# Optimization experiments

Hardware: AMD Instinct MI355X
Metric: run time of the kernel (lower is better)

Reference implementation:

```python
import jax, jax.numpy as jnp
import numpy as np

B, T, D, H, K = 4, 2048, 512, 8, 31
INNER = 2048  # dim * ff_mult
DH = D // H   # 64
EPS = 1e-5

def _ln(x, g, b):
    m = jnp.mean(x, axis=-1, keepdims=True)
    v = jnp.var(x, axis=-1, keepdims=True)
    return (x - m) * jax.lax.rsqrt(v + EPS) * g + b

def _ff(x, g, b, w1, b1, w2, b2):
    h = jax.nn.silu(_ln(x, g, b) @ w1 + b1)
    return h @ w2 + b2

def _rope_cos_sin(t, dh, theta=10000.0):
    freqs = 1.0 / theta ** (jnp.arange(0, dh, 2, dtype=jnp.float32) / dh)
    ang = jnp.arange(t, dtype=jnp.float32)[:, None] * freqs[None, :]
    return jnp.cos(ang), jnp.sin(ang)

def _rotate(x, cos, sin):
    # x: [B,T,H,DH]; complex rotation on (even, odd) pairs, matches torch view_as_complex
    xr = x.reshape(x.shape[:-1] + (DH // 2, 2))
    xe, xo = xr[..., 0], xr[..., 1]
    c, s = cos[None, :, None, :], sin[None, :, None, :]
    return jnp.stack([xe * c - xo * s, xe * s + xo * c], axis=-1).reshape(x.shape)

def setup_inputs():
    ks = iter(jax.random.split(jax.random.key(0), 16))
    w = lambda *s: jax.random.normal(next(ks), s, jnp.float32) * 0.02
    ones = lambda n: jnp.ones((n,), jnp.float32)
    zeros = lambda n: jnp.zeros((n,), jnp.float32)
    return dict(
        x=jax.random.normal(next(ks), (B, T, D), jnp.float32),
        ff1_lng=ones(D), ff1_lnb=zeros(D),
        ff1_w1=w(D, INNER), ff1_b1=zeros(INNER), ff1_w2=w(INNER, D), ff1_b2=zeros(D),
        attn_lng=ones(D), attn_lnb=zeros(D),
        wq=w(D, D), wk=w(D, D), wv=w(D, D), wo=w(D, D),
        conv_lng=ones(D), conv_lnb=zeros(D),
        pw1_w=w(D, 2 * D), pw1_b=zeros(2 * D),
        dw_w=w(D, K), dw_b=zeros(D),
        bn_g=ones(D), bn_b=zeros(D),
        pw2_w=w(D, D), pw2_b=zeros(D),
        ff2_lng=ones(D), ff2_lnb=zeros(D),
        ff2_w1=w(D, INNER), ff2_b1=zeros(INNER), ff2_w2=w(INNER, D), ff2_b2=zeros(D),
        out_lng=ones(D), out_lnb=zeros(D),
    )

def reference(x, ff1_lng, ff1_lnb, ff1_w1, ff1_b1, ff1_w2, ff1_b2,
              attn_lng, attn_lnb, wq, wk, wv, wo,
              conv_lng, conv_lnb, pw1_w, pw1_b, dw_w, dw_b, bn_g, bn_b, pw2_w, pw2_b,
              ff2_lng, ff2_lnb, ff2_w1, ff2_b1, ff2_w2, ff2_b2,
              out_lng, out_lnb):
    # ff1 half-step
    x = x + 0.5 * _ff(x, ff1_lng, ff1_lnb, ff1_w1, ff1_b1, ff1_w2, ff1_b2)
    # RoPE MHSA
    h = _ln(x, attn_lng, attn_lnb)
    q = (h @ wq).reshape(B, T, H, DH)
    k = (h @ wk).reshape(B, T, H, DH)
    v = (h @ wv).reshape(B, T, H, DH)
    cos, sin = _rope_cos_sin(T, DH)
    q, k = _rotate(q, cos, sin), _rotate(k, cos, sin)
    scores = jnp.einsum('bqhd,bkhd->bhqk', q, k) / np.float32(np.sqrt(DH))
    o = jnp.einsum('bhqk,bkhd->bqhd', jax.nn.softmax(scores, axis=-1), v).reshape(B, T, D)
    x = x + o @ wo
    # Conformer conv module
    h = _ln(x, conv_lng, conv_lnb) @ pw1_w + pw1_b         # pointwise1 -> [B,T,2D]
    h = h[..., :D] * jax.nn.sigmoid(h[..., D:])            # GLU over channels
    h = h.transpose(0, 2, 1)                               # [B,D,T]
    h = jax.lax.conv_general_dilated(h, dw_w[:, None, :], (1,), [(K // 2, K // 2)],
                                     dimension_numbers=('NCH', 'OIH', 'NCH'),
                                     feature_group_count=D) + dw_b[None, :, None]
    mu = jnp.mean(h, axis=(0, 2), keepdims=True)           # training-mode BatchNorm1d
    var = jnp.var(h, axis=(0, 2), keepdims=True)
    h = (h - mu) * jax.lax.rsqrt(var + EPS) * bn_g[None, :, None] + bn_b[None, :, None]
    h = jax.nn.silu(h).transpose(0, 2, 1) @ pw2_w + pw2_b  # pointwise2 -> [B,T,D]
    x = x + h
    # ff2 half-step + final LN
    x = x + 0.5 * _ff(x, ff2_lng, ff2_lnb, ff2_w1, ff2_b1, ff2_w2, ff2_b2)
    return _ln(x, out_lng, out_lnb)
```

## Files before the change

kernel.cpp:

```cpp
#include <hip/hip_runtime.h>


typedef float  f32x4   __attribute__((ext_vector_type(4)));
typedef float  f32x16  __attribute__((ext_vector_type(16)));
typedef __bf16 bf16_t;
typedef __bf16 bf16x8  __attribute__((ext_vector_type(8)));
typedef unsigned short u16;
typedef unsigned short u16x4 __attribute__((ext_vector_type(4)));
typedef unsigned short u16x8 __attribute__((ext_vector_type(8)));
typedef unsigned int   u32x4 __attribute__((ext_vector_type(4)));

#define DEVI __device__ __forceinline__

static constexpr int CB = 4, CT = 2048, CD = 512, CH = 8, CDH = 64, CINNER = 2048, CK = 31;
static constexpr int CBT = CB * CT;

DEVI u16 f2bf(float f) {
  unsigned u = __builtin_bit_cast(unsigned, f);
  u += 0x7FFFu + ((u >> 16) & 1u);
  return (u16)(u >> 16);
}
DEVI float bf2f(u16 h) { return __builtin_bit_cast(float, (unsigned)h << 16); }
DEVI float sigm(float x) { return 1.0f / (1.0f + __expf(-x)); }

DEVI unsigned cvtpk(float lo, float hi) {
  unsigned r;
  asm("v_cvt_pk_bf16_f32 %0, %1, %2" : "=v"(r) : "v"(lo), "v"(hi));
  return r;
}

DEVI void gload16(const bf16_t* g, bf16_t* l) {
  __builtin_amdgcn_global_load_lds(
      (const __attribute__((address_space(1))) unsigned int*)g,
      (__attribute__((address_space(3))) unsigned int*)l, 16, 0, 0);
}

DEVI void pipe_wait(int t, int nt) {
  if (t + 3 <= nt)      asm volatile("s_waitcnt vmcnt(12)" ::: "memory");
  else if (t + 2 == nt) asm volatile("s_waitcnt vmcnt(6)" ::: "memory");
  else                  asm volatile("s_waitcnt vmcnt(0)" ::: "memory");
}

enum { EPI_BF = 0, EPI_SILU_BF = 1, EPI_RES = 2, EPI_GLU = 3 };

template<int EPI>
__global__ __launch_bounds__(512) void gemm8(
    const bf16_t* __restrict__ A, const bf16_t* __restrict__ B,
    const float* __restrict__ bias, const float* __restrict__ res,
    void* __restrict__ Cv,
    int lda, int ldb, int ldc, int Kd, float scale)
{
  __shared__ __align__(16) bf16_t As[3][256 * 64];
  __shared__ __align__(16) bf16_t Bs[3][128 * 64];

  const int gx = gridDim.x;
  const int nwg = gx * gridDim.y;
  int wg = blockIdx.y * gx + blockIdx.x;
  wg = (wg & 7) * (nwg >> 3) + (wg >> 3);
  const int m0 = (wg / gx) * 256, n0 = (wg % gx) * 128;

  const int tid = threadIdx.x;
  const int wid = tid >> 6, lane = tid & 63;
  const int lrow = lane & 15, lk = lane >> 4;
  const int wm = (wid >> 1) * 64, wn = (wid & 1) * 64;
  const int r = tid >> 3;
  const int cs = (((tid & 7) ^ (r & 7)) << 3);
  const int fsw = lrow & 7;

  auto stage = [&](int kt, int s) {
    const bf16_t* ga = A + (long)(m0 + r) * lda + (kt * 64 + cs);
    const bf16_t* gb = B + (long)(n0 + r) * ldb + (kt * 64 + cs);
    bf16_t* as = &As[s][0];
    bf16_t* bs = &Bs[s][0];
#pragma unroll
    for (int it = 0; it < 4; ++it)
      gload16(ga + (long)it * 64 * lda, as + tid * 8 + it * 4096);
#pragma unroll
    for (int it = 0; it < 2; ++it)
      gload16(gb + (long)it * 64 * ldb, bs + tid * 8 + it * 4096);
  };

  f32x4 acc[4][4] = {};
  const int nt = Kd / 64;

  stage(0, 0);
  stage(1, 1);
  stage(2, 2);

  int s = 0;
  for (int t = 0; t < nt; ++t) {
    pipe_wait(t, nt);
    asm volatile("s_barrier" ::: "memory");

    bf16x8 av[2][4], bv[2][4];
    const bf16_t* as = &As[s][0];
    const bf16_t* bs = &Bs[s][0];
#pragma unroll
    for (int kk = 0; kk < 2; ++kk) {
#pragma unroll
      for (int i = 0; i < 4; ++i)
        av[kk][i] = *(const bf16x8*)&as[(wm + i * 16 + lrow) * 64 + ((((kk << 2) + lk) ^ fsw) << 3)];
#pragma unroll
      for (int j = 0; j < 4; ++j)
        bv[kk][j] = *(const bf16x8*)&bs[(wn + j * 16 + lrow) * 64 + ((((kk << 2) + lk) ^ fsw) << 3)];
    }
    __builtin_amdgcn_s_setprio(1);
#pragma unroll
    for (int kk = 0; kk < 2; ++kk)
#pragma unroll
      for (int i = 0; i < 4; ++i)
#pragma unroll
        for (int j = 0; j < 4; ++j)
          acc[i][j] = __builtin_amdgcn_mfma_f32_16x16x32_bf16(av[kk][i], bv[kk][j], acc[i][j], 0, 0, 0);
    __builtin_amdgcn_s_setprio(0);

    asm volatile("s_barrier" ::: "memory");
    if (t + 3 < nt) stage(t + 3, s);
    s = (s == 2) ? 0 : s + 1;
  }

  if constexpr (EPI == EPI_GLU) {
#pragma unroll
    for (int jp = 0; jp < 2; ++jp) {
      int oc = ((n0 + wn) >> 1) + jp * 16 + lrow;
      float ba = bias[oc], bb = bias[512 + oc];
#pragma unroll
      for (int i = 0; i < 4; ++i) {
#pragma unroll
        for (int rr = 0; rr < 4; ++rr) {
          int row = m0 + wm + i * 16 + lk * 4 + rr;
          float av_ = acc[i][2 * jp][rr] + ba;
          float bv_ = acc[i][2 * jp + 1][rr] + bb;
          ((bf16_t*)Cv)[(long)row * ldc + oc] = (bf16_t)(av_ * sigm(bv_));
        }
      }
    }
  } else {
#pragma unroll
    for (int j = 0; j < 4; ++j) {
      int col = n0 + wn + j * 16 + lrow;
      float bb = bias ? bias[col] : 0.0f;
#pragma unroll
      for (int i = 0; i < 4; ++i) {
#pragma unroll
        for (int rr = 0; rr < 4; ++rr) {
          int row = m0 + wm + i * 16 + lk * 4 + rr;
          long idx = (long)row * ldc + col;
          float v = (acc[i][j][rr] + bb) * scale;
          if constexpr (EPI == EPI_SILU_BF) v *= sigm(v);
          if constexpr (EPI == EPI_RES) {
            ((float*)Cv)[idx] = res[idx] + v;
          } else {
            ((bf16_t*)Cv)[idx] = (bf16_t)v;
          }
        }
      }
    }
  }
}

template<int BM, int BN, int BK, int EPI>
__global__ __launch_bounds__(256) void gemm_bf(
    const bf16_t* __restrict__ A, const bf16_t* __restrict__ B,
    const float* __restrict__ bias, const float* __restrict__ res,
    void* __restrict__ Cv,
    int lda, int ldb, int ldc, int Kd, float scale)
{
  __shared__ __align__(16) bf16_t As[BM * BK];
  __shared__ __align__(16) bf16_t Bs[BN * BK];

  const int gx = gridDim.x;
  const int nwg = gx * gridDim.y;
  int wg = blockIdx.y * gx + blockIdx.x;
  wg = (wg & 7) * (nwg >> 3) + (wg >> 3);
  const int m0 = (wg / gx) * BM, n0 = (wg % gx) * BN;

  const int tid = threadIdx.x;
  const int wid = tid >> 6, lane = tid & 63;
  const int lrow = lane & 15, lk = lane >> 4;
  constexpr int FM = BM / 32, FN = BN / 32;
  constexpr int NK = BK / 32;
  constexpr int TPR = BK / 8;
  constexpr int RPP = 256 / TPR;
  const int wm = (wid >> 1) * (BM / 2), wn = (wid & 1) * (BN / 2);
  const int r = tid / TPR;
  const int cs = (((tid & (TPR - 1)) ^ (r & 7)) << 3);
  const int fsw = lrow & 7;

  f32x4 acc[FM][FN] = {};

  for (int k0 = 0; k0 < Kd; k0 += BK) {
    const bf16_t* ga = A + (long)(m0 + r) * lda + (k0 + cs);
    const bf16_t* gb = B + (long)(n0 + r) * ldb + (k0 + cs);
#pragma unroll
    for (int it = 0; it < BM / RPP; ++it)
      gload16(ga + (long)it * RPP * lda, &As[tid * 8 + it * 2048]);
#pragma unroll
    for (int it = 0; it < BN / RPP; ++it)
      gload16(gb + (long)it * RPP * ldb, &Bs[tid * 8 + it * 2048]);
    __syncthreads();

    bf16x8 av[NK][FM], bv[NK][FN];
#pragma unroll
    for (int kk = 0; kk < NK; ++kk) {
#pragma unroll
      for (int i = 0; i < FM; ++i)
        av[kk][i] = *(const bf16x8*)&As[(wm + i * 16 + lrow) * BK + ((((kk << 2) + lk) ^ fsw) << 3)];
#pragma unroll
      for (int j = 0; j < FN; ++j)
        bv[kk][j] = *(const bf16x8*)&Bs[(wn + j * 16 + lrow) * BK + ((((kk << 2) + lk) ^ fsw) << 3)];
    }
#pragma unroll
    for (int kk = 0; kk < NK; ++kk)
#pragma unroll
      for (int i = 0; i < FM; ++i)
#pragma unroll
        for (int j = 0; j < FN; ++j)
          acc[i][j] = __builtin_amdgcn_mfma_f32_16x16x32_bf16(av[kk][i], bv[kk][j], acc[i][j], 0, 0, 0);
    __syncthreads();
  }

#pragma unroll
  for (int j = 0; j < FN; ++j) {
    int col = n0 + wn + j * 16 + lrow;
    float bb = bias ? bias[col] : 0.0f;
#pragma unroll
    for (int i = 0; i < FM; ++i) {
#pragma unroll
      for (int rr = 0; rr < 4; ++rr) {
        int row = m0 + wm + i * 16 + lk * 4 + rr;
        long idx = (long)row * ldc + col;
        float v = (acc[i][j][rr] + bb) * scale;
        if constexpr (EPI == EPI_SILU_BF) v *= sigm(v);
        if constexpr (EPI == EPI_RES) {
          ((float*)Cv)[idx] = res[idx] + v;
        } else {
          ((bf16_t*)Cv)[idx] = (bf16_t)v;
        }
      }
    }
  }
}

__global__ __launch_bounds__(256) void fattn_k(
    const bf16_t* __restrict__ QK,
    const bf16_t* __restrict__ VT,
    bf16_t* __restrict__ O)
{
  __shared__ __align__(16) bf16_t S[16384];

  const int tid = threadIdx.x;
  const int w = tid >> 6, lane = tid & 63;
  const int l31 = lane & 31, hi = lane >> 5;
  const int q0 = blockIdx.x * 128;
  const int bh = blockIdx.y, b = bh >> 3, h = bh & 7;

  const int r8 = tid >> 3;
  const int csw = ((tid & 7) ^ (r8 & 7)) << 3;
  const int fswl = l31 & 7;

  const bf16_t* Qg = QK + ((long)b * CT + q0) * 1536 + h * 64;
  const bf16_t* Kg = QK + (long)b * CT * 1536 + 512 + h * 64;
  const bf16_t* Vg = VT + (long)bh * 64 * 2048;

#pragma unroll
  for (int it = 0; it < 4; ++it)
    gload16(Qg + (long)(r8 + it * 32) * 1536 + csw, &S[8192 + tid * 8 + it * 2048]);
#pragma unroll
  for (int it = 0; it < 2; ++it)
    gload16(Kg + (long)(r8 + it * 32) * 1536 + csw, &S[tid * 8 + it * 2048]);
#pragma unroll
  for (int it = 0; it < 2; ++it)
    gload16(Vg + (long)(r8 + it * 32) * 2048 + csw, &S[4096 + tid * 8 + it * 2048]);
  __syncthreads();

  bf16x8 qb[4];
#pragma unroll
  for (int m = 0; m < 4; ++m)
    qb[m] = *(const bf16x8*)&S[8192 + (w * 32 + l31) * 64 + (((m * 2 + hi) ^ fswl) << 3)];
  __syncthreads();

  const u16x8 onesu = {0x3F80, 0x3F80, 0x3F80, 0x3F80, 0x3F80, 0x3F80, 0x3F80, 0x3F80};
  const bf16x8 onesf = __builtin_bit_cast(bf16x8, onesu);

  f32x16 o0 = {}, o1 = {}, lacc = {};
  float mrun = -3.0e38f;

#define FA_BODY(CURK, CURV, NXTK, NXTV, KV0, STG)                               \
  {                                                                             \
    if (STG) {                                                                  \
      const int nxt = (KV0) + 64;                                               \
      _Pragma("unroll")                                                         \
      for (int it = 0; it < 2; ++it)                                            \
        gload16(Kg + (long)(nxt + r8 + it * 32) * 1536 + csw,                   \
                &S[(NXTK) + tid * 8 + it * 2048]);                              \
      _Pragma("unroll")                                                         \
      for (int it = 0; it < 2; ++it)                                            \
        gload16(Vg + (long)(r8 + it * 32) * 2048 + nxt + csw,                   \
                &S[(NXTV) + tid * 8 + it * 2048]);                              \
    }                                                                           \
    bf16x8 ka[2][4];                                                            \
    _Pragma("unroll")                                                           \
    for (int j = 0; j < 2; ++j)                                                 \
      _Pragma("unroll")                                                         \
      for (int m = 0; m < 4; ++m)                                               \
        ka[j][m] = *(const bf16x8*)&S[(CURK) + (j * 32 + l31) * 64 +            \
                                      (((m * 2 + hi) ^ fswl) << 3)];            \
    f32x16 s0 = {}, s1 = {};                                                    \
    __builtin_amdgcn_s_setprio(1);                                              \
    _Pragma("unroll")                                                           \
    for (int m = 0; m < 4; ++m) {                                               \
      s0 = __builtin_amdgcn_mfma_f32_32x32x16_bf16(ka[0][m], qb[m], s0, 0, 0, 0); \
      s1 = __builtin_amdgcn_mfma_f32_32x32x16_bf16(ka[1][m], qb[m], s1, 0, 0, 0); \
    }                                                                           \
    __builtin_amdgcn_s_setprio(0);                                              \
    float tm[16];                                                               \
    _Pragma("unroll")                                                           \
    for (int rr = 0; rr < 16; ++rr) tm[rr] = fmaxf(s0[rr], s1[rr]);             \
    _Pragma("unroll")                                                           \
    for (int stp = 8; stp; stp >>= 1)                                           \
      _Pragma("unroll")                                                         \
      for (int rr = 0; rr < stp; ++rr) tm[rr] = fmaxf(tm[rr], tm[rr + stp]);    \
    float pm = tm[0];                                                           \
    { float pa = pm, pb = pm;                                                   \
      asm("v_permlane32_swap_b32 %0, %1" : "+v"(pa), "+v"(pb));                 \
      pm = fmaxf(pa, pb); }                                                     \
    if (!__all(pm <= mrun + 8.0f)) {                                            \
      float mn = fmaxf(mrun, pm);                                               \
      float al = exp2f(mrun - mn);                                              \
      mrun = mn;                                                                \
      lacc[0] *= al;                                                            \
      _Pragma("unroll")                                                         \
      for (int rr = 0; rr < 16; ++rr) { o0[rr] *= al; o1[rr] *= al; }           \
    }                                                                           \
    _Pragma("unroll")                                                           \
    for (int rr = 0; rr < 16; ++rr) s0[rr] = exp2f(s0[rr] - mrun);              \
    _Pragma("unroll")                                                           \
    for (int rr = 0; rr < 16; ++rr) s1[rr] = exp2f(s1[rr] - mrun);              \
    bf16x8 pw[4];                                                               \
    _Pragma("unroll")                                                           \
    for (int jk = 0; jk < 4; ++jk) {                                            \
      float e0, e1, e2, e3, e4, e5, e6, e7;                                     \
      if (jk == 0) { e0=s0[0];e1=s0[1];e2=s0[2];e3=s0[3];e4=s0[4];e5=s0[5];e6=s0[6];e7=s0[7]; }        \
      else if (jk == 1) { e0=s0[8];e1=s0[9];e2=s0[10];e3=s0[11];e4=s0[12];e5=s0[13];e6=s0[14];e7=s0[15]; } \
      else if (jk == 2) { e0=s1[0];e1=s1[1];e2=s1[2];e3=s1[3];e4=s1[4];e5=s1[5];e6=s1[6];e7=s1[7]; }   \
      else { e0=s1[8];e1=s1[9];e2=s1[10];e3=s1[11];e4=s1[12];e5=s1[13];e6=s1[14];e7=s1[15]; }          \
      unsigned a0 = cvtpk(e0, e1), a1 = cvtpk(e2, e3);                          \
      unsigned b0 = cvtpk(e4, e5), b1 = cvtpk(e6, e7);                          \
      asm("v_permlane32_swap_b32 %0, %1" : "+v"(a0), "+v"(b0));                 \
      asm("v_permlane32_swap_b32 %0, %1" : "+v"(a1), "+v"(b1));                 \
      u32x4 t; t[0] = a0; t[1] = a1; t[2] = b0; t[3] = b1;                      \
      pw[jk] = __builtin_bit_cast(bf16x8, t);                                   \
    }                                                                           \
    bf16x8 va[2][4];                                                            \
    _Pragma("unroll")                                                           \
    for (int n = 0; n < 2; ++n)                                                 \
      _Pragma("unroll")                                                         \
      for (int jk = 0; jk < 4; ++jk)                                            \
        va[n][jk] = *(const bf16x8*)&S[(CURV) + (n * 32 + l31) * 64 +           \
                                       (((jk * 2 + hi) ^ fswl) << 3)];          \
    __builtin_amdgcn_s_setprio(1);                                              \
    _Pragma("unroll")                                                           \
    for (int jk = 0; jk < 4; ++jk) {                                            \
      o0 = __builtin_amdgcn_mfma_f32_32x32x16_bf16(va[0][jk], pw[jk], o0, 0, 0, 0); \
      o1 = __builtin_amdgcn_mfma_f32_32x32x16_bf16(va[1][jk], pw[jk], o1, 0, 0, 0); \
      lacc = __builtin_amdgcn_mfma_f32_32x32x16_bf16(onesf, pw[jk], lacc, 0, 0, 0); \
    }                                                                           \
    __builtin_amdgcn_s_setprio(0);                                              \
    __syncthreads();                                                            \
  }

  for (int kv0 = 0; kv0 < CT; kv0 += 128) {
    FA_BODY(0, 4096, 8192, 12288, kv0, 1)
    FA_BODY(8192, 12288, 0, 4096, kv0 + 64, (kv0 + 128 < CT))
  }
#undef FA_BODY

  float rl = 1.0f / lacc[0];
  bf16_t* Op = O + ((long)b * CT + q0 + w * 32 + l31) * CD + h * 64;
#pragma unroll
  for (int n = 0; n < 2; ++n) {
#pragma unroll
    for (int m = 0; m < 4; ++m) {
      u16x4 pk4;
#pragma unroll
      for (int e = 0; e < 4; ++e)
        pk4[e] = f2bf((n ? o1[m * 4 + e] : o0[m * 4 + e]) * rl);
      *(u16x4*)(Op + n * 32 + m * 8 + hi * 4) = pk4;
    }
  }
}

__global__ __launch_bounds__(256) void wtrans_k(
    const float* __restrict__ w, u16* __restrict__ o, int Kd, int N)
{
  __shared__ u16 lt[64][72];
  const int k0 = blockIdx.y * 64, n0 = blockIdx.x * 64;
  const int tid = threadIdx.x;
#pragma unroll
  for (int it = 0; it < 4; ++it) {
    int kk = (tid >> 4) + it * 16, nn = (tid & 15) * 4;
    float4 f = *(const float4*)(w + (long)(k0 + kk) * N + n0 + nn);
    lt[kk][nn + 0] = f2bf(f.x); lt[kk][nn + 1] = f2bf(f.y);
    lt[kk][nn + 2] = f2bf(f.z); lt[kk][nn + 3] = f2bf(f.w);
  }
  __syncthreads();
#pragma unroll
  for (int it = 0; it < 2; ++it) {
    int nn = (tid >> 3) + it * 32, kk = (tid & 7) * 8;
    u16x8 pk;
#pragma unroll
    for (int e = 0; e < 8; ++e) pk[e] = lt[kk + e][nn];
    *(u16x8*)(o + (long)(n0 + nn) * Kd + k0 + kk) = pk;
  }
}

__global__ __launch_bounds__(256) void pwtrans_k(
    const float* __restrict__ w, u16* __restrict__ o)
{
  __shared__ u16 lt[64][72];
  const int k0 = blockIdx.y * 64, n0 = blockIdx.x * 64;
  const int tid = threadIdx.x;
#pragma unroll
  for (int it = 0; it < 4; ++it) {
    int kk = (tid >> 4) + it * 16, nn = (tid & 15) * 4;
    float4 f = *(const float4*)(w + (long)(k0 + kk) * 1024 + n0 + nn);
    lt[kk][nn + 0] = f2bf(f.x); lt[kk][nn + 1] = f2bf(f.y);
    lt[kk][nn + 2] = f2bf(f.z); lt[kk][nn + 3] = f2bf(f.w);
  }
  __syncthreads();
#pragma unroll
  for (int it = 0; it < 2; ++it) {
    int nn = (tid >> 3) + it * 32, kk = (tid & 7) * 8;
    int s = n0 + nn;
    int d = ((s & 511) >> 4) * 32 + (s >> 9) * 16 + (s & 15);
    u16x8 pk;
#pragma unroll
    for (int e = 0; e < 8; ++e) pk[e] = lt[kk + e][nn];
    *(u16x8*)(o + (long)d * 512 + k0 + kk) = pk;
  }
}

__global__ __launch_bounds__(256) void vtrans_k(
    const u16* __restrict__ v, u16* __restrict__ vt)
{
  __shared__ u16 lt[64][72];
  const int bh = blockIdx.y, b = bh >> 3, h = bh & 7;
  const int t0 = blockIdx.x * 64;
  const int tid = threadIdx.x;
#pragma unroll
  for (int it = 0; it < 2; ++it) {
    int tt = (tid >> 3) + it * 32, dd = (tid & 7) * 8;
    u16x8 vv = *(const u16x8*)(v + ((long)b * CT + t0 + tt) * 1536 + 1024 + h * 64 + dd);
#pragma unroll
    for (int e = 0; e < 8; ++e) lt[tt][dd + e] = vv[e];
  }
  __syncthreads();
#pragma unroll
  for (int it = 0; it < 2; ++it) {
    int dd = (tid >> 3) + it * 32, tt = (tid & 7) * 8;
    u16x8 pk;
#pragma unroll
    for (int e = 0; e < 8; ++e) pk[e] = lt[tt + e][dd];
    *(u16x8*)(vt + ((long)bh * 64 + dd) * CT + t0 + tt) = pk;
  }
}

__global__ void dwt_k(const float* __restrict__ w, float* __restrict__ o)
{
  int i = blockIdx.x * 256 + threadIdx.x;
  if (i < 512 * 31) { int c = i / 31, k = i % 31; o[k * 512 + c] = w[i]; }
}

template<int OBF>
__global__ __launch_bounds__(256) void ln_k(
    const float* __restrict__ in, const float* __restrict__ g,
    const float* __restrict__ b, void* __restrict__ out)
{
  __shared__ float rs[4], rq[4];
  const long row = blockIdx.x;
  const int tid = threadIdx.x;
  float2 v = ((const float2*)(in + row * CD))[tid];
  float s = v.x + v.y, q = v.x * v.x + v.y * v.y;
#pragma unroll
  for (int o = 32; o; o >>= 1) { s += __shfl_xor(s, o); q += __shfl_xor(q, o); }
  if ((tid & 63) == 0) { rs[tid >> 6] = s; rq[tid >> 6] = q; }
  __syncthreads();
  s = rs[0] + rs[1] + rs[2] + rs[3];
  q = rq[0] + rq[1] + rq[2] + rq[3];
  float mean = s * (1.0f / CD);
  float var = q * (1.0f / CD) - mean * mean;
  float rstd = rsqrtf(var + 1e-5f);
  float2 gg = ((const float2*)g)[tid];
  float2 bb = ((const float2*)b)[tid];
  float ox = (v.x - mean) * rstd * gg.x + bb.x;
  float oy = (v.y - mean) * rstd * gg.y + bb.y;
  if (OBF) {
    unsigned pk = ((unsigned)f2bf(oy) << 16) | f2bf(ox);
    ((unsigned*)out)[row * 256 + tid] = pk;
  } else {
    ((float2*)out)[row * 256 + tid] = make_float2(ox, oy);
  }
}

__global__ void rope_table_k(float* __restrict__ cosT, float* __restrict__ sinT)
{
  int tid = blockIdx.x * 256 + threadIdx.x;
  int t = tid >> 5, i = tid & 31;
  float freq = __expf(-(float)i * (9.210340371976184f / 32.0f));
  float ang = (float)t * freq;
  cosT[tid] = cosf(ang);
  sinT[tid] = sinf(ang);
}

__global__ __launch_bounds__(256) void rope_k(
    unsigned* __restrict__ qkv,
    const float* __restrict__ cosT, const float* __restrict__ sinT)
{
  const float SC = 0.125f * 1.44269504089f;
  long p = (long)blockIdx.x * 256 + threadIdx.x;
  int pr = (int)(p & 255);
  long row = p >> 8;
  int t = (int)(row & (CT - 1));
  int h = pr >> 5, i = pr & 31;
  float c = cosT[t * 32 + i], s = sinT[t * 32 + i];
  unsigned* base = qkv + row * 768 + h * 32 + i;
  unsigned v = base[0];
  float xe = bf2f((u16)v), xo = bf2f((u16)(v >> 16));
  base[0] = ((unsigned)f2bf((xe * s + xo * c) * SC) << 16) | f2bf((xe * c - xo * s) * SC);
  v = base[256];
  xe = bf2f((u16)v); xo = bf2f((u16)(v >> 16));
  base[256] = ((unsigned)f2bf(xe * s + xo * c) << 16) | f2bf(xe * c - xo * s);
}

__global__ __launch_bounds__(256) void dwconv_k(
    const u16* __restrict__ in, const float* __restrict__ wT,
    const float* __restrict__ wb, u16* __restrict__ out)
{
  long idx = (long)blockIdx.x * 256 + threadIdx.x;
  int c4 = (int)(idx & 127) * 4;
  int t0 = (int)((idx >> 7) & 255) * 8;
  int b = (int)(idx >> 15);
  const u16* base = in + (long)b * CT * CD;
  float4 bias = *(const float4*)(wb + c4);
  float4 acc[8];
#pragma unroll
  for (int t = 0; t < 8; ++t) acc[t] = bias;
#pragma unroll
  for (int j = 0; j < 38; ++j) {
    int tr = t0 + j - 15;
    float4 row = make_float4(0.f, 0.f, 0.f, 0.f);
    if (tr >= 0 && tr < CT) {
      u16x4 rv = *(const u16x4*)(base + (long)tr * CD + c4);
      row = make_float4(bf2f(rv[0]), bf2f(rv[1]), bf2f(rv[2]), bf2f(rv[3]));
    }
#pragma unroll
    for (int t = 0; t < 8; ++t) {
      int k = j - t;
      if (k >= 0 && k < CK) {
        float4 w4 = *(const float4*)(wT + k * CD + c4);
        acc[t].x += row.x * w4.x; acc[t].y += row.y * w4.y;
        acc[t].z += row.z * w4.z; acc[t].w += row.w * w4.w;
      }
    }
  }
#pragma unroll
  for (int t = 0; t < 8; ++t) {
    u16x4 pk;
    pk[0] = f2bf(acc[t].x); pk[1] = f2bf(acc[t].y);
    pk[2] = f2bf(acc[t].z); pk[3] = f2bf(acc[t].w);
    *(u16x4*)(out + ((long)b * CT + t0 + t) * CD + c4) = pk;
  }
}

__global__ __launch_bounds__(256) void bn_part_k(
    const u16* __restrict__ in, float* __restrict__ psum, float* __restrict__ psq)
{
  const int blk = blockIdx.x;
  const int tid = threadIdx.x;
  const int c0 = tid, c1 = tid + 256;
  const int rows = CBT / 256;
  const u16* base = in + (long)blk * rows * CD;
  float s0 = 0, q0 = 0, s1 = 0, q1 = 0;
  for (int r = 0; r < rows; ++r) {
    float v0 = bf2f(base[(long)r * CD + c0]); s0 += v0; q0 += v0 * v0;
    float v1 = bf2f(base[(long)r * CD + c1]); s1 += v1; q1 += v1 * v1;
  }
  psum[blk * CD + c0] = s0; psq[blk * CD + c0] = q0;
  psum[blk * CD + c1] = s1; psq[blk * CD + c1] = q1;
}

__global__ __launch_bounds__(256) void bn_fin_k(
    const float* __restrict__ psum, const float* __restrict__ psq,
    float* __restrict__ stat)
{
  int c = blockIdx.x * 256 + threadIdx.x;
  float s = 0, q = 0;
  for (int i = 0; i < 256; ++i) { s += psum[i * CD + c]; q += psq[i * CD + c]; }
  float mean = s * (1.0f / CBT);
  float var = q * (1.0f / CBT) - mean * mean;
  stat[c] = mean;
  stat[CD + c] = rsqrtf(var + 1e-5f);
}

__global__ __launch_bounds__(256) void bn_app_k(
    const u16* __restrict__ h, const float* __restrict__ stat,
    const float* __restrict__ g, const float* __restrict__ b,
    u16* __restrict__ out)
{
  long idx = (long)blockIdx.x * 256 + threadIdx.x;
  int c = (int)(idx & 511);
  float v = (bf2f(h[idx]) - stat[c]) * stat[CD + c] * g[c] + b[c];
  v = v * sigm(v);
  out[idx] = f2bf(v);
}

extern "C" void kernel_launch(void* const* d_in, const int* in_sizes, int n_in,
                              void* d_out, int out_size, void* d_ws, size_t ws_size,
                              hipStream_t stream)
{
  const float* x        = (const float*)d_in[0];
  const float* ff1_lng  = (const float*)d_in[1];
  const float* ff1_lnb  = (const float*)d_in[2];
  const float* ff1_w1   = (const float*)d_in[3];
  const float* ff1_b1   = (const float*)d_in[4];
  const float* ff1_w2   = (const float*)d_in[5];
  const float* ff1_b2   = (const float*)d_in[6];
  const float* attn_lng = (const float*)d_in[7];
  const float* attn_lnb = (const float*)d_in[8];
  const float* wq       = (const float*)d_in[9];
  const float* wk       = (const float*)d_in[10];
  const float* wv       = (const float*)d_in[11];
  const float* wo       = (const float*)d_in[12];
  const float* conv_lng = (const float*)d_in[13];
  const float* conv_lnb = (const float*)d_in[14];
  const float* pw1_w    = (const float*)d_in[15];
  const float* pw1_b    = (const float*)d_in[16];
  const float* dw_w     = (const float*)d_in[17];
  const float* dw_b     = (const float*)d_in[18];
  const float* bn_g     = (const float*)d_in[19];
  const float* bn_b     = (const float*)d_in[20];
  const float* pw2_w    = (const float*)d_in[21];
  const float* pw2_b    = (const float*)d_in[22];
  const float* ff2_lng  = (const float*)d_in[23];
  const float* ff2_lnb  = (const float*)d_in[24];
  const float* ff2_w1   = (const float*)d_in[25];
  const float* ff2_b1   = (const float*)d_in[26];
  const float* ff2_w2   = (const float*)d_in[27];
  const float* ff2_b2   = (const float*)d_in[28];
  const float* out_lng  = (const float*)d_in[29];
  const float* out_lnb  = (const float*)d_in[30];
  float* out = (float*)d_out;

  char* p = (char*)d_ws;
  auto alloc = [&](size_t bytes) { char* r = p; p += (bytes + 255) & ~(size_t)255; return r; };
  float*  bufX   = (float*)alloc((size_t)CBT * CD * 4);
  bf16_t* bufH   = (bf16_t*)alloc((size_t)CBT * CD * 2);
  bf16_t* bufQKV = (bf16_t*)alloc((size_t)CBT * 1536 * 2);
  bf16_t* bufO   = (bf16_t*)alloc((size_t)CBT * CD * 2);
  bf16_t* bufVT  = (bf16_t*)alloc((size_t)CBT * CD * 2);
  bf16_t* bufP   = (bf16_t*)alloc((size_t)CBT * CINNER * 2);
  bf16_t* w_ff1a = (bf16_t*)alloc((size_t)CD * CINNER * 2);
  bf16_t* w_ff1b = (bf16_t*)alloc((size_t)CD * CINNER * 2);
  bf16_t* w_qkv  = (bf16_t*)alloc((size_t)CD * 1536 * 2);
  bf16_t* w_o    = (bf16_t*)alloc((size_t)CD * CD * 2);
  bf16_t* w_pw1  = (bf16_t*)alloc((size_t)CD * 2 * CD * 2);
  bf16_t* w_pw2  = (bf16_t*)alloc((size_t)CD * CD * 2);
  bf16_t* w_ff2a = (bf16_t*)alloc((size_t)CD * CINNER * 2);
  bf16_t* w_ff2b = (bf16_t*)alloc((size_t)CD * CINNER * 2);
  float* dwT  = (float*)alloc((size_t)CK * CD * 4);
  float* cosT = (float*)alloc((size_t)CT * 32 * 4);
  float* sinT = (float*)alloc((size_t)CT * 32 * 4);
  float* psum = (float*)alloc((size_t)256 * CD * 4);
  float* psq  = (float*)alloc((size_t)256 * CD * 4);
  float* stat = (float*)alloc((size_t)2 * CD * 4);

  const dim3 blk(256);
  const dim3 blk8(512);

  wtrans_k<<<dim3(CINNER / 64, CD / 64), blk, 0, stream>>>(ff1_w1, (u16*)w_ff1a, CD, CINNER);
  wtrans_k<<<dim3(CD / 64, CINNER / 64), blk, 0, stream>>>(ff1_w2, (u16*)w_ff1b, CINNER, CD);
  wtrans_k<<<dim3(CD / 64, CD / 64), blk, 0, stream>>>(wq, (u16*)w_qkv, CD, CD);
  wtrans_k<<<dim3(CD / 64, CD / 64), blk, 0, stream>>>(wk, (u16*)(w_qkv + (size_t)512 * CD), CD, CD);
  wtrans_k<<<dim3(CD / 64, CD / 64), blk, 0, stream>>>(wv, (u16*)(w_qkv + (size_t)1024 * CD), CD, CD);
  wtrans_k<<<dim3(CD / 64, CD / 64), blk, 0, stream>>>(wo, (u16*)w_o, CD, CD);
  pwtrans_k<<<dim3(1024 / 64, CD / 64), blk, 0, stream>>>(pw1_w, (u16*)w_pw1);
  wtrans_k<<<dim3(CD / 64, CD / 64), blk, 0, stream>>>(pw2_w, (u16*)w_pw2, CD, CD);
  wtrans_k<<<dim3(CINNER / 64, CD / 64), blk, 0, stream>>>(ff2_w1, (u16*)w_ff2a, CD, CINNER);
  wtrans_k<<<dim3(CD / 64, CINNER / 64), blk, 0, stream>>>(ff2_w2, (u16*)w_ff2b, CINNER, CD);
  dwt_k<<<dim3(62), blk, 0, stream>>>(dw_w, dwT);
  rope_table_k<<<dim3(CT * 32 / 256), blk, 0, stream>>>(cosT, sinT);

  ln_k<1><<<dim3(CBT), blk, 0, stream>>>(x, ff1_lng, ff1_lnb, bufH);
  gemm8<EPI_SILU_BF><<<dim3(16, 32), blk8, 0, stream>>>(
      bufH, w_ff1a, ff1_b1, nullptr, bufP, CD, CD, CINNER, CD, 1.0f);
  gemm_bf<64, 128, 128, EPI_RES><<<dim3(4, 128), blk, 0, stream>>>(
      bufP, w_ff1b, ff1_b2, x, bufX, CINNER, CINNER, CD, CINNER, 0.5f);

  ln_k<1><<<dim3(CBT), blk, 0, stream>>>(bufX, attn_lng, attn_lnb, bufH);
  gemm8<EPI_BF><<<dim3(12, 32), blk8, 0, stream>>>(
      bufH, w_qkv, nullptr, nullptr, bufQKV, CD, CD, 1536, CD, 1.0f);
  rope_k<<<dim3(CB * CT), blk, 0, stream>>>((unsigned*)bufQKV, cosT, sinT);
  vtrans_k<<<dim3(CT / 64, CB * CH), blk, 0, stream>>>((const u16*)bufQKV, (u16*)bufVT);
  fattn_k<<<dim3(CT / 128, CB * CH), blk, 0, stream>>>(bufQKV, bufVT, bufO);
  gemm_bf<64, 128, 128, EPI_RES><<<dim3(4, 128), blk, 0, stream>>>(
      bufO, w_o, nullptr, bufX, bufX, CD, CD, CD, CD, 1.0f);

  ln_k<1><<<dim3(CBT), blk, 0, stream>>>(bufX, conv_lng, conv_lnb, bufH);
  gemm8<EPI_GLU><<<dim3(8, 32), blk8, 0, stream>>>(
      bufH, w_pw1, pw1_b, nullptr, bufH, CD, CD, CD, CD, 1.0f);
  dwconv_k<<<dim3(512), blk, 0, stream>>>((const u16*)bufH, dwT, dw_b, (u16*)bufO);
  bn_part_k<<<dim3(256), blk, 0, stream>>>((const u16*)bufO, psum, psq);
  bn_fin_k<<<dim3(2), blk, 0, stream>>>(psum, psq, stat);
  bn_app_k<<<dim3(CBT * CD / 256), blk, 0, stream>>>((const u16*)bufO, stat, bn_g, bn_b, (u16*)bufH);
  gemm_bf<64, 128, 128, EPI_RES><<<dim3(4, 128), blk, 0, stream>>>(
      bufH, w_pw2, pw2_b, bufX, bufX, CD, CD, CD, CD, 1.0f);

  ln_k<1><<<dim3(CBT), blk, 0, stream>>>(bufX, ff2_lng, ff2_lnb, bufH);
  gemm8<EPI_SILU_BF><<<dim3(16, 32), blk8, 0, stream>>>(
      bufH, w_ff2a, ff2_b1, nullptr, bufP, CD, CD, CINNER, CD, 1.0f);
  gemm_bf<64, 128, 128, EPI_RES><<<dim3(4, 128), blk, 0, stream>>>(
      bufP, w_ff2b, ff2_b2, bufX, bufX, CINNER, CINNER, CD, CINNER, 0.5f);

  ln_k<0><<<dim3(CBT), blk, 0, stream>>>(bufX, out_lng, out_lnb, out);

  (void)in_sizes; (void)n_in; (void)out_size; (void)ws_size;
}
```

Before: 389.1 us.

## Fuse V transpose into QKV GEMM, BN stats into dwconv, use raw exp2

The QKV GEMM epilogue now writes V directly in transposed [b,h,d,t] layout, which removes the separate vtrans kernel. BatchNorm partial sums are computed inside the depthwise conv kernel and combined with atomics, which removes the bn_part pass over the conv output and shrinks bn_fin to a direct read. Attention softmax uses a raw v_exp_f32 inline asm instead of exp2f. The trade-offs are scattered 8-byte V stores, atomic contention on 512 counters, float-atomic ordering nondeterminism, and loss of exp2f's denormal handling.

```diff
diff --git a/kernel.cpp b/kernel.cpp
--- a/kernel.cpp
+++ b/kernel.cpp
@@ -23,6 +23,12 @@
 DEVI float bf2f(u16 h) { return __builtin_bit_cast(float, (unsigned)h << 16); }
 DEVI float sigm(float x) { return 1.0f / (1.0f + __expf(-x)); }
 
+DEVI float fex2(float x) {
+  float r;
+  asm("v_exp_f32 %0, %1\n\ts_nop 1" : "=v"(r) : "v"(x));
+  return r;
+}
+
 DEVI unsigned cvtpk(float lo, float hi) {
   unsigned r;
   asm("v_cvt_pk_bf16_f32 %0, %1, %2" : "=v"(r) : "v"(lo), "v"(hi));
@@ -41,7 +47,7 @@
   else                  asm volatile("s_waitcnt vmcnt(0)" ::: "memory");
 }
 
-enum { EPI_BF = 0, EPI_SILU_BF = 1, EPI_RES = 2, EPI_GLU = 3 };
+enum { EPI_BF = 0, EPI_SILU_BF = 1, EPI_RES = 2, EPI_GLU = 3, EPI_QKV = 4 };
 
 template<int EPI>
 __global__ __launch_bounds__(512) void gemm8(
@@ -132,6 +138,34 @@
           float av_ = acc[i][2 * jp][rr] + ba;
           float bv_ = acc[i][2 * jp + 1][rr] + bb;
           ((bf16_t*)Cv)[(long)row * ldc + oc] = (bf16_t)(av_ * sigm(bv_));
+        }
+      }
+    }
+  } else if constexpr (EPI == EPI_QKV) {
+    bf16_t* vt = (bf16_t*)res;
+#pragma unroll
+    for (int j = 0; j < 4; ++j) {
+      int col = n0 + wn + j * 16 + lrow;
+      if (col < 1024) {
+#pragma unroll
+        for (int i = 0; i < 4; ++i) {
+#pragma unroll
+          for (int rr = 0; rr < 4; ++rr) {
+            int row = m0 + wm + i * 16 + lk * 4 + rr;
+            ((bf16_t*)Cv)[(long)row * ldc + col] = (bf16_t)acc[i][j][rr];
+          }
+        }
+      } else {
+        int dg = col - 1024;
+        int hh = dg >> 6, d = dg & 63;
+#pragma unroll
+        for (int i = 0; i < 4; ++i) {
+          int row0 = m0 + wm + i * 16 + lk * 4;
+          int b = row0 >> 11, t = row0 & 2047;
+          u16x4 pk;
+#pragma unroll
+          for (int rr = 0; rr < 4; ++rr) pk[rr] = f2bf(acc[i][j][rr]);
+          *(u16x4*)(vt + ((long)(b * 8 + hh) * 64 + d) * 2048 + t) = pk;
         }
       }
     }
@@ -327,16 +361,16 @@
       pm = fmaxf(pa, pb); }                                                     \
     if (!__all(pm <= mrun + 8.0f)) {                                            \
       float mn = fmaxf(mrun, pm);                                               \
-      float al = exp2f(mrun - mn);                                              \
+      float al = fex2(mrun - mn);                                               \
       mrun = mn;                                                                \
       lacc[0] *= al;                                                            \
       _Pragma("unroll")                                                         \
       for (int rr = 0; rr < 16; ++rr) { o0[rr] *= al; o1[rr] *= al; }           \
     }                                                                           \
     _Pragma("unroll")                                                           \
-    for (int rr = 0; rr < 16; ++rr) s0[rr] = exp2f(s0[rr] - mrun);              \
-    _Pragma("unroll")                                                           \
-    for (int rr = 0; rr < 16; ++rr) s1[rr] = exp2f(s1[rr] - mrun);              \
+    for (int rr = 0; rr < 16; ++rr) s0[rr] = fex2(s0[rr] - mrun);               \
+    _Pragma("unroll")                                                           \
+    for (int rr = 0; rr < 16; ++rr) s1[rr] = fex2(s1[rr] - mrun);               \
     bf16x8 pw[4];                                                               \
     _Pragma("unroll")                                                           \
     for (int jk = 0; jk < 4; ++jk) {                                            \
@@ -438,31 +472,6 @@
 #pragma unroll
     for (int e = 0; e < 8; ++e) pk[e] = lt[kk + e][nn];
     *(u16x8*)(o + (long)d * 512 + k0 + kk) = pk;
-  }
-}
-
-__global__ __launch_bounds__(256) void vtrans_k(
-    const u16* __restrict__ v, u16* __restrict__ vt)
-{
-  __shared__ u16 lt[64][72];
-  const int bh = blockIdx.y, b = bh >> 3, h = bh & 7;
-  const int t0 = blockIdx.x * 64;
-  const int tid = threadIdx.x;
-#pragma unroll
-  for (int it = 0; it < 2; ++it) {
-    int tt = (tid >> 3) + it * 32, dd = (tid & 7) * 8;
-    u16x8 vv = *(const u16x8*)(v + ((long)b * CT + t0 + tt) * 1536 + 1024 + h * 64 + dd);
-#pragma unroll
-    for (int e = 0; e < 8; ++e) lt[tt][dd + e] = vv[e];
-  }
-  __syncthreads();
-#pragma unroll
-  for (int it = 0; it < 2; ++it) {
-    int dd = (tid >> 3) + it * 32, tt = (tid & 7) * 8;
-    u16x8 pk;
-#pragma unroll
-    for (int e = 0; e < 8; ++e) pk[e] = lt[tt + e][dd];
-    *(u16x8*)(vt + ((long)bh * 64 + dd) * CT + t0 + tt) = pk;
   }
 }
 
@@ -535,9 +544,12 @@
 
 __global__ __launch_bounds__(256) void dwconv_k(
     const u16* __restrict__ in, const float* __restrict__ wT,
-    const float* __restrict__ wb, u16* __restrict__ out)
-{
+    const float* __restrict__ wb, u16* __restrict__ out,
+    float* __restrict__ psum, float* __restrict__ psq)
+{
+  __shared__ float ls[128][8];
   long idx = (long)blockIdx.x * 256 + threadIdx.x;
+  const int tid = threadIdx.x;
   int c4 = (int)(idx & 127) * 4;
   int t0 = (int)((idx >> 7) & 255) * 8;
   int b = (int)(idx >> 15);
@@ -564,30 +576,30 @@
       }
     }
   }
+  float s4[4] = {}, q4[4] = {};
 #pragma unroll
   for (int t = 0; t < 8; ++t) {
     u16x4 pk;
     pk[0] = f2bf(acc[t].x); pk[1] = f2bf(acc[t].y);
     pk[2] = f2bf(acc[t].z); pk[3] = f2bf(acc[t].w);
     *(u16x4*)(out + ((long)b * CT + t0 + t) * CD + c4) = pk;
-  }
-}
-
-__global__ __launch_bounds__(256) void bn_part_k(
-    const u16* __restrict__ in, float* __restrict__ psum, float* __restrict__ psq)
-{
-  const int blk = blockIdx.x;
-  const int tid = threadIdx.x;
-  const int c0 = tid, c1 = tid + 256;
-  const int rows = CBT / 256;
-  const u16* base = in + (long)blk * rows * CD;
-  float s0 = 0, q0 = 0, s1 = 0, q1 = 0;
-  for (int r = 0; r < rows; ++r) {
-    float v0 = bf2f(base[(long)r * CD + c0]); s0 += v0; q0 += v0 * v0;
-    float v1 = bf2f(base[(long)r * CD + c1]); s1 += v1; q1 += v1 * v1;
-  }
-  psum[blk * CD + c0] = s0; psq[blk * CD + c0] = q0;
-  psum[blk * CD + c1] = s1; psq[blk * CD + c1] = q1;
+    s4[0] += acc[t].x; q4[0] += acc[t].x * acc[t].x;
+    s4[1] += acc[t].y; q4[1] += acc[t].y * acc[t].y;
+    s4[2] += acc[t].z; q4[2] += acc[t].z * acc[t].z;
+    s4[3] += acc[t].w; q4[3] += acc[t].w * acc[t].w;
+  }
+  if (tid >= 128) {
+#pragma unroll
+    for (int e = 0; e < 4; ++e) { ls[tid - 128][e] = s4[e]; ls[tid - 128][4 + e] = q4[e]; }
+  }
+  __syncthreads();
+  if (tid < 128) {
+#pragma unroll
+    for (int e = 0; e < 4; ++e) {
+      atomicAdd(&psum[c4 + e], s4[e] + ls[tid][e]);
+      atomicAdd(&psq[c4 + e],  q4[e] + ls[tid][4 + e]);
+    }
+  }
 }
 
 __global__ __launch_bounds__(256) void bn_fin_k(
@@ -595,8 +607,7 @@
     float* __restrict__ stat)
 {
   int c = blockIdx.x * 256 + threadIdx.x;
-  float s = 0, q = 0;
-  for (int i = 0; i < 256; ++i) { s += psum[i * CD + c]; q += psq[i * CD + c]; }
+  float s = psum[c], q = psq[c];
   float mean = s * (1.0f / CBT);
   float var = q * (1.0f / CBT) - mean * mean;
   stat[c] = mean;
@@ -671,8 +682,8 @@
   float* dwT  = (float*)alloc((size_t)CK * CD * 4);
   float* cosT = (float*)alloc((size_t)CT * 32 * 4);
   float* sinT = (float*)alloc((size_t)CT * 32 * 4);
-  float* psum = (float*)alloc((size_t)256 * CD * 4);
-  float* psq  = (float*)alloc((size_t)256 * CD * 4);
+  float* psum = (float*)alloc((size_t)CD * 4);
+  float* psq  = (float*)alloc((size_t)CD * 4);
   float* stat = (float*)alloc((size_t)2 * CD * 4);
 
   const dim3 blk(256);
@@ -690,6 +701,8 @@
   wtrans_k<<<dim3(CD / 64, CINNER / 64), blk, 0, stream>>>(ff2_w2, (u16*)w_ff2b, CINNER, CD);
   dwt_k<<<dim3(62), blk, 0, stream>>>(dw_w, dwT);
   rope_table_k<<<dim3(CT * 32 / 256), blk, 0, stream>>>(cosT, sinT);
+  hipMemsetAsync(psum, 0, (size_t)CD * 4, stream);
+  hipMemsetAsync(psq, 0, (size_t)CD * 4, stream);
 
   ln_k<1><<<dim3(CBT), blk, 0, stream>>>(x, ff1_lng, ff1_lnb, bufH);
   gemm8<EPI_SILU_BF><<<dim3(16, 32), blk8, 0, stream>>>(
@@ -698,10 +711,9 @@
       bufP, w_ff1b, ff1_b2, x, bufX, CINNER, CINNER, CD, CINNER, 0.5f);
 
   ln_k<1><<<dim3(CBT), blk, 0, stream>>>(bufX, attn_lng, attn_lnb, bufH);
-  gemm8<EPI_BF><<<dim3(12, 32), blk8, 0, stream>>>(
-      bufH, w_qkv, nullptr, nullptr, bufQKV, CD, CD, 1536, CD, 1.0f);
+  gemm8<EPI_QKV><<<dim3(12, 32), blk8, 0, stream>>>(
+      bufH, w_qkv, nullptr, (const float*)bufVT, bufQKV, CD, CD, 1536, CD, 1.0f);
   rope_k<<<dim3(CB * CT), blk, 0, stream>>>((unsigned*)bufQKV, cosT, sinT);
-  vtrans_k<<<dim3(CT / 64, CB * CH), blk, 0, stream>>>((const u16*)bufQKV, (u16*)bufVT);
   fattn_k<<<dim3(CT / 128, CB * CH), blk, 0, stream>>>(bufQKV, bufVT, bufO);
   gemm_bf<64, 128, 128, EPI_RES><<<dim3(4, 128), blk, 0, stream>>>(
       bufO, w_o, nullptr, bufX, bufX, CD, CD, CD, CD, 1.0f);
@@ -709,8 +721,7 @@
   ln_k<1><<<dim3(CBT), blk, 0, stream>>>(bufX, conv_lng, conv_lnb, bufH);
   gemm8<EPI_GLU><<<dim3(8, 32), blk8, 0, stream>>>(
       bufH, w_pw1, pw1_b, nullptr, bufH, CD, CD, CD, CD, 1.0f);
-  dwconv_k<<<dim3(512), blk, 0, stream>>>((const u16*)bufH, dwT, dw_b, (u16*)bufO);
-  bn_part_k<<<dim3(256), blk, 0, stream>>>((const u16*)bufO, psum, psq);
+  dwconv_k<<<dim3(512), blk, 0, stream>>>((const u16*)bufH, dwT, dw_b, (u16*)bufO, psum, psq);
   bn_fin_k<<<dim3(2), blk, 0, stream>>>(psum, psq, stat);
   bn_app_k<<<dim3(CBT * CD / 256), blk, 0, stream>>>((const u16*)bufO, stat, bn_g, bn_b, (u16*)bufH);
   gemm_bf<64, 128, 128, EPI_RES><<<dim3(4, 128), blk, 0, stream>>>(
```

After: 399.7 us. 2.7% more time.
